# Kernel tuning notes

Hardware: AMD Instinct MI355X
Metric: run time of the kernel (lower is better)

The kernel has to match this reference:

```python
import jax, jax.numpy as jnp
import numpy as np

N = 128       # SSM state size
L = 32768     # l_max / sequence length
DT_MIN, DT_MAX = 0.001, 0.1


def setup_inputs() -> dict:
    key = jax.random.key(0)
    ku, ka, kb, kc, ks = jax.random.split(key, 5)
    u = jax.random.normal(ku, (L,), dtype=jnp.float32)
    # lecun_normal: std = 1/sqrt(fan_in); shift A by -2I for stability over L powers
    A = jax.random.normal(ka, (N, N), dtype=jnp.float32) * (1.0 / np.sqrt(N)) - 2.0 * jnp.eye(N, dtype=jnp.float32)
    B = jax.random.normal(kb, (N, 1), dtype=jnp.float32)            # fan_in=1 -> std 1
    C = jax.random.normal(kc, (1, N), dtype=jnp.float32) * (1.0 / np.sqrt(N))
    D = jnp.ones((1,), dtype=jnp.float32)
    log_step = jax.random.uniform(ks, (1,), dtype=jnp.float32) * (np.log(DT_MAX) - np.log(DT_MIN)) + np.log(DT_MIN)
    return {"u": u, "A": A, "B": B, "C": C, "D": D, "log_step": log_step}


def discretize(a, b, step):
    # bilinear (Tustin) discretization, identical to the flax module
    i = jnp.eye(a.shape[0], dtype=a.dtype)
    bl = jnp.linalg.inv(i - (step / 2.0) * a)
    ab = bl @ (i + (step / 2.0) * a)
    bb = (bl * step) @ b
    return ab, bb


def k_conv(ab, bb, cb, l):
    # K[t] = cb @ ab^t @ bb  -- same math as the matrix_power list-comp,
    # computed with a single scan carrying x_t = ab^t @ bb  (N,1)
    def step(x, _):
        k_t = (cb @ x).reshape(())
        return ab @ x, k_t
    _, k = jax.lax.scan(step, bb, None, length=l)
    return k  # (l,)


def causal_convolution(u, k):
    l = u.shape[0]
    ud = jnp.fft.rfft(jnp.pad(u, (0, k.shape[0])))
    kd = jnp.fft.rfft(jnp.pad(k, (0, l)))
    return jnp.fft.irfft(ud * kd)[:l]


def reference(u, A, B, C, D, log_step):
    step = jnp.exp(log_step)
    ab, bb = discretize(A, B, step)
    K = k_conv(ab, bb, C, u.shape[0])
    return causal_convolution(u, K) + D * u
```

## Files before the change

### kernel.cpp

```cpp
#include <hip/hip_runtime.h>
#include <math.h>

#define L_SEQ 32768
#define NS 128
#define TS 2048

__global__ __launch_bounds__(256) void build_T(const float* __restrict__ A,
                                               const float* __restrict__ lstep,
                                               float* __restrict__ T,
                                               float* __restrict__ U1) {
  int idx = blockIdx.x * 256 + threadIdx.x;
  if (idx >= NS * NS) return;
  int i = idx >> 7, j = idx & 127;
  float step = expf(lstep[0]);
  float alpha = 0.5f * step / (1.0f + step);
  float g = A[idx] + ((i == j) ? 2.0f : 0.0f);
  float t = alpha * g;
  T[idx] = t;
  U1[idx] = t + ((i == j) ? 1.0f : 0.0f);
}

__global__ __launch_bounds__(256) void gemm2(
    const float* __restrict__ A1, const float* __restrict__ B1, float* __restrict__ C1,
    int M1, int lgP1, int ldb1, int ldc1, int mode1,
    const float* __restrict__ A2, const float* __restrict__ B2, float* __restrict__ C2,
    int M2, int lgP2, int ldb2, int ldc2, int mode2,
    int n1, const float* __restrict__ lstep) {
  int b = blockIdx.x;
  bool sec = (b >= n1);
  const float* Ap = sec ? A2 : A1;
  const float* Bp = sec ? B2 : B1;
  float* Cp = sec ? C2 : C1;
  int M   = sec ? M2 : M1;
  int lgP = sec ? lgP2 : lgP1;
  int ldb = sec ? ldb2 : ldb1;
  int ldc = sec ? ldc2 : ldc1;
  int mode = sec ? mode2 : mode1;
  int bid = sec ? (b - n1) : b;

  int idx = bid * 256 + threadIdx.x;
  int total = M << lgP;
  if (idx >= total) return;
  int i = idx >> lgP;
  int j = idx & ((1 << lgP) - 1);

  const float* Arow = Ap + i * NS;
  float acc = 0.f;
#pragma unroll 8
  for (int k = 0; k < NS; ++k) acc = fmaf(Arow[k], Bp[k * ldb + j], acc);

  float out;
  if (mode == 0) {
    out = acc;
  } else if (mode == 1) {
    out = acc + Arow[j];
  } else if (mode == 2) {
    out = acc + Arow[j] + Bp[i * ldb + j] + ((i == j) ? 1.f : 0.f);
  } else {
    float step = expf(lstep[0]);
    out = (2.f / (1.f + step)) * acc - ((i == j) ? 1.f : 0.f);
  }
  Cp[i * ldc + j] = out;
}

__global__ __launch_bounds__(256) void prep(const float* __restrict__ ab,
                                            const float* __restrict__ B,
                                            const float* __restrict__ C,
                                            const float* __restrict__ lstep,
                                            float* __restrict__ R,
                                            float* __restrict__ S) {
  int t = threadIdx.x;
  if (t < NS) {
    float acc = 0.f;
    for (int k = 0; k < NS; ++k) acc = fmaf(ab[t * NS + k], B[k], acc);
    float step = expf(lstep[0]);
    R[t * 256] = 0.5f * step * (acc + B[t]);
  } else if (t < 2 * NS) {
    int j = t - NS;
    S[j] = C[j];
  }
}

__global__ __launch_bounds__(256) void conv_partial(const float* __restrict__ u,
                                                    const float* __restrict__ Kv,
                                                    float* __restrict__ Pp) {
  __shared__ __align__(16) float ks[TS];
  __shared__ __align__(16) float us[2 * TS];

  int bid = blockIdx.x;
  int m = 0;
  while ((m + 1) * (m + 2) / 2 <= bid) m++;
  int c = bid - m * (m + 1) / 2;
  int w0 = (m - c) * TS - TS;
  int tid = threadIdx.x;

  for (int idx = tid; idx < TS; idx += 256) ks[idx] = Kv[c * TS + idx];
  for (int idx = tid; idx < 2 * TS; idx += 256) {
    int gi = w0 + idx;
    us[idx] = (gi >= 0) ? u[gi] : 0.f;
  }
  __syncthreads();

  float acc[8];
#pragma unroll
  for (int i = 0; i < 8; ++i) acc[i] = 0.f;

  int tb = tid << 3;

  for (int s8 = 0; s8 < TS; s8 += 8) {
    float4 k0 = *(const float4*)&ks[s8];
    float4 k1 = *(const float4*)&ks[s8 + 4];
    int base = TS + tb - s8;
    float4 ua = *(const float4*)&us[base - 8];
    float4 ub = *(const float4*)&us[base - 4];
    float4 uc = *(const float4*)&us[base];
    float4 ud = *(const float4*)&us[base + 4];
    float w[16] = {ua.x, ua.y, ua.z, ua.w, ub.x, ub.y, ub.z, ub.w,
                   uc.x, uc.y, uc.z, uc.w, ud.x, ud.y, ud.z, ud.w};
    float kk[8] = {k0.x, k0.y, k0.z, k0.w, k1.x, k1.y, k1.z, k1.w};
#pragma unroll
    for (int ds = 0; ds < 8; ++ds) {
#pragma unroll
      for (int i = 0; i < 8; ++i) acc[i] = fmaf(kk[ds], w[8 + i - ds], acc[i]);
    }
  }

  float* dst = Pp + c * L_SEQ + m * TS + tb;
  *(float4*)&dst[0] = make_float4(acc[0], acc[1], acc[2], acc[3]);
  *(float4*)&dst[4] = make_float4(acc[4], acc[5], acc[6], acc[7]);
}

__global__ __launch_bounds__(256) void reduce_k(const float* __restrict__ Pp,
                                                const float* __restrict__ u,
                                                const float* __restrict__ D,
                                                float* __restrict__ y) {
  int t = blockIdx.x * 256 + threadIdx.x;
  if (t >= L_SEQ) return;
  int mmax = t >> 11;
  float acc = D[0] * u[t];
  for (int c = 0; c <= mmax; ++c) acc += Pp[c * L_SEQ + t];
  y[t] = acc;
}

static inline void launch_gemm1(hipStream_t s, const float* A, const float* B, float* C,
                                int M, int lgP, int ldb, int ldc, int mode,
                                const float* lstep) {
  int n1 = ((M << lgP) + 255) >> 8;
  hipLaunchKernelGGL(gemm2, dim3(n1), dim3(256), 0, s,
                     A, B, C, M, lgP, ldb, ldc, mode,
                     (const float*)nullptr, (const float*)nullptr, (float*)nullptr,
                     0, 0, 0, 0, 0, n1, lstep);
}

static inline void launch_gemm2j(hipStream_t s,
                                 const float* A1, const float* B1, float* C1,
                                 int M1, int lgP1, int ldb1, int ldc1, int mode1,
                                 const float* A2, const float* B2, float* C2,
                                 int M2, int lgP2, int ldb2, int ldc2, int mode2,
                                 const float* lstep) {
  int n1 = ((M1 << lgP1) + 255) >> 8;
  int n2 = ((M2 << lgP2) + 255) >> 8;
  hipLaunchKernelGGL(gemm2, dim3(n1 + n2), dim3(256), 0, s,
                     A1, B1, C1, M1, lgP1, ldb1, ldc1, mode1,
                     A2, B2, C2, M2, lgP2, ldb2, ldc2, mode2, n1, lstep);
}

extern "C" void kernel_launch(void* const* d_in, const int* in_sizes, int n_in,
                              void* d_out, int out_size, void* d_ws, size_t ws_size,
                              hipStream_t stream) {
  (void)in_sizes; (void)n_in; (void)out_size; (void)ws_size;
  const float* u     = (const float*)d_in[0];
  const float* A     = (const float*)d_in[1];
  const float* B     = (const float*)d_in[2];
  const float* C     = (const float*)d_in[3];
  const float* D     = (const float*)d_in[4];
  const float* lstep = (const float*)d_in[5];
  float* y  = (float*)d_out;
  float* ws = (float*)d_ws;

  float* T   = ws + 0;
  float* U1  = ws + 16384;
  float* T2  = ws + 32768;
  float* T4  = ws + 49152;
  float* T8  = ws + 65536;
  float* U12 = ws + 81920;
  float* U48 = ws + 98304;
  float* ab  = ws + 114688;
  float* pwA = ws + 131072;
  float* pwB = ws + 147456;
  float* R   = ws + 163840;
  float* S   = ws + 196608;
  float* Kv  = ws + 212992;
  float* Pp  = ws + 245760;

  hipLaunchKernelGGL(build_T, dim3(64), dim3(256), 0, stream, A, lstep, T, U1);
  launch_gemm1(stream, T, T, T2, 128, 7, 128, 128, 0, lstep);
  launch_gemm2j(stream, T2, T2, T4, 128, 7, 128, 128, 0,
                U1, T2, U12, 128, 7, 128, 128, 1, lstep);
  launch_gemm1(stream, T4, T4, T8, 128, 7, 128, 128, 0, lstep);
  launch_gemm1(stream, T4, T8, U48, 128, 7, 128, 128, 2, lstep);
  launch_gemm1(stream, U12, U48, ab, 128, 7, 128, 128, 3, lstep);
  hipLaunchKernelGGL(prep, dim3(1), dim3(256), 0, stream, ab, B, C, lstep, R, S);

  auto pw = [&](int k) -> float* { return k == 0 ? ab : ((k & 1) ? pwA : pwB); };

  for (int k = 0; k < 8; ++k) {
    launch_gemm2j(stream, pw(k), R, R + (1 << k), 128, k, 256, 256, 0,
                  pw(k), pw(k), pw(k + 1), 128, 7, 128, 128, 0, lstep);
  }
  for (int k = 0; k < 7; ++k) {
    if (k < 6) {
      launch_gemm2j(stream, S, pw(8 + k), S + (1 << k) * 128, 1 << k, 7, 128, 128, 0,
                    pw(8 + k), pw(8 + k), pw(9 + k), 128, 7, 128, 128, 0, lstep);
    } else {
      launch_gemm1(stream, S, pw(8 + k), S + (1 << k) * 128, 1 << k, 7, 128, 128, 0, lstep);
    }
  }

  launch_gemm1(stream, S, R, Kv, 128, 8, 256, 256, 0, lstep);

  hipLaunchKernelGGL(conv_partial, dim3(136), dim3(256), 0, stream, u, Kv, Pp);
  hipLaunchKernelGGL(reduce_k, dim3(128), dim3(256), 0, stream, Pp, u, D, y);
}
```

Baseline: 245.9 us.

## Fuse matrix-power chain into one persistent kernel with grid barriers; retile convolution

Replaces the roughly twenty small GEMM launches that build the discretized matrix, its powers and the kernel vector with one persistent 128-block kernel. The stages are separated by atomic-counter grid barriers, so per-launch overhead and inter-kernel gaps go away. The block convolution drops from 2048 to 1024 tiles (528 blocks, four outputs per thread) and uses an XOR-swizzled shared-memory layout for u with a register-rotating window. The grid barrier assumes all 128 blocks are co-resident, and the reduce step now sums more partial blocks per output.

New measurement: 277.7 us. 1.13x slower.

```diff
diff --git a/kernel.cpp b/kernel.cpp
--- a/kernel.cpp
+++ b/kernel.cpp
@@ -2,132 +2,205 @@
 #include <math.h>
 
 #define L_SEQ 32768
-#define NS 128
-#define TS 2048
-
-__global__ __launch_bounds__(256) void build_T(const float* __restrict__ A,
+#define NBLK 128
+
+__device__ __forceinline__ void gbar(int* cnt, int target) {
+  __syncthreads();
+  if (threadIdx.x == 0) {
+    __hip_atomic_fetch_add(cnt, 1, __ATOMIC_RELEASE, __HIP_MEMORY_SCOPE_AGENT);
+    while (__hip_atomic_load(cnt, __ATOMIC_ACQUIRE, __HIP_MEMORY_SCOPE_AGENT) < target) {
+      __builtin_amdgcn_s_sleep(2);
+    }
+  }
+  __syncthreads();
+}
+
+__device__ __forceinline__ float dot128(const float* __restrict__ Ar,
+                                        const float* __restrict__ B,
+                                        int ldb, int j) {
+  float a0 = 0.f, a1 = 0.f, a2 = 0.f, a3 = 0.f;
+#pragma unroll
+  for (int k = 0; k < 128; k += 4) {
+    a0 = fmaf(Ar[k],     B[(k)     * ldb + j], a0);
+    a1 = fmaf(Ar[k + 1], B[(k + 1) * ldb + j], a1);
+    a2 = fmaf(Ar[k + 2], B[(k + 2) * ldb + j], a2);
+    a3 = fmaf(Ar[k + 3], B[(k + 3) * ldb + j], a3);
+  }
+  return (a0 + a1) + (a2 + a3);
+}
+
+__global__ __launch_bounds__(256) void chain_k(const float* __restrict__ A,
+                                               const float* __restrict__ Bv,
+                                               const float* __restrict__ Cv,
                                                const float* __restrict__ lstep,
-                                               float* __restrict__ T,
-                                               float* __restrict__ U1) {
-  int idx = blockIdx.x * 256 + threadIdx.x;
-  if (idx >= NS * NS) return;
-  int i = idx >> 7, j = idx & 127;
+                                               float* ws) {
+  int* cnt   = (int*)ws;
+  float* T   = ws + 16;
+  float* U1  = T   + 16384;
+  float* T2  = U1  + 16384;
+  float* T4  = T2  + 16384;
+  float* T8  = T4  + 16384;
+  float* U12 = T8  + 16384;
+  float* U48 = U12 + 16384;
+  float* ab  = U48 + 16384;
+  float* pwA = ab  + 16384;
+  float* pwB = pwA + 16384;
+  float* R   = pwB + 16384;
+  float* S   = R   + 32768;
+  float* Kv  = S   + 16384;
+
+  int tid = blockIdx.x * 256 + threadIdx.x;
   float step = expf(lstep[0]);
-  float alpha = 0.5f * step / (1.0f + step);
-  float g = A[idx] + ((i == j) ? 2.0f : 0.0f);
-  float t = alpha * g;
-  T[idx] = t;
-  U1[idx] = t + ((i == j) ? 1.0f : 0.0f);
-}
-
-__global__ __launch_bounds__(256) void gemm2(
-    const float* __restrict__ A1, const float* __restrict__ B1, float* __restrict__ C1,
-    int M1, int lgP1, int ldb1, int ldc1, int mode1,
-    const float* __restrict__ A2, const float* __restrict__ B2, float* __restrict__ C2,
-    int M2, int lgP2, int ldb2, int ldc2, int mode2,
-    int n1, const float* __restrict__ lstep) {
-  int b = blockIdx.x;
-  bool sec = (b >= n1);
-  const float* Ap = sec ? A2 : A1;
-  const float* Bp = sec ? B2 : B1;
-  float* Cp = sec ? C2 : C1;
-  int M   = sec ? M2 : M1;
-  int lgP = sec ? lgP2 : lgP1;
-  int ldb = sec ? ldb2 : ldb1;
-  int ldc = sec ? ldc2 : ldc1;
-  int mode = sec ? mode2 : mode1;
-  int bid = sec ? (b - n1) : b;
-
-  int idx = bid * 256 + threadIdx.x;
-  int total = M << lgP;
-  if (idx >= total) return;
-  int i = idx >> lgP;
-  int j = idx & ((1 << lgP) - 1);
-
-  const float* Arow = Ap + i * NS;
-  float acc = 0.f;
-#pragma unroll 8
-  for (int k = 0; k < NS; ++k) acc = fmaf(Arow[k], Bp[k * ldb + j], acc);
-
-  float out;
-  if (mode == 0) {
-    out = acc;
-  } else if (mode == 1) {
-    out = acc + Arow[j];
-  } else if (mode == 2) {
-    out = acc + Arow[j] + Bp[i * ldb + j] + ((i == j) ? 1.f : 0.f);
+  int bar = 0;
+
+  if (tid < 16384) {
+    int i = tid >> 7, j = tid & 127;
+    float alpha = 0.5f * step / (1.0f + step);
+    float g = A[tid] + ((i == j) ? 2.0f : 0.0f);
+    float t = alpha * g;
+    T[tid] = t;
+    U1[tid] = t + ((i == j) ? 1.0f : 0.0f);
+  }
+  gbar(cnt, NBLK * (++bar));
+
+  if (tid < 16384) {
+    int i = tid >> 7, j = tid & 127;
+    T2[tid] = dot128(T + i * 128, T, 128, j);
+  }
+  gbar(cnt, NBLK * (++bar));
+
+  if (tid < 16384) {
+    int i = tid >> 7, j = tid & 127;
+    T4[tid] = dot128(T2 + i * 128, T2, 128, j);
   } else {
-    float step = expf(lstep[0]);
-    out = (2.f / (1.f + step)) * acc - ((i == j) ? 1.f : 0.f);
-  }
-  Cp[i * ldc + j] = out;
-}
-
-__global__ __launch_bounds__(256) void prep(const float* __restrict__ ab,
-                                            const float* __restrict__ B,
-                                            const float* __restrict__ C,
-                                            const float* __restrict__ lstep,
-                                            float* __restrict__ R,
-                                            float* __restrict__ S) {
-  int t = threadIdx.x;
-  if (t < NS) {
+    int t2 = tid - 16384;
+    int i = t2 >> 7, j = t2 & 127;
+    U12[t2] = dot128(U1 + i * 128, T2, 128, j) + U1[t2];
+  }
+  gbar(cnt, NBLK * (++bar));
+
+  if (tid < 16384) {
+    int i = tid >> 7, j = tid & 127;
+    T8[tid] = dot128(T4 + i * 128, T4, 128, j);
+  }
+  gbar(cnt, NBLK * (++bar));
+
+  if (tid < 16384) {
+    int i = tid >> 7, j = tid & 127;
+    U48[tid] = dot128(T4 + i * 128, T8, 128, j) + T4[tid] + T8[tid] +
+               ((i == j) ? 1.f : 0.f);
+  }
+  gbar(cnt, NBLK * (++bar));
+
+  if (tid < 16384) {
+    int i = tid >> 7, j = tid & 127;
+    ab[tid] = (2.f / (1.f + step)) * dot128(U12 + i * 128, U48, 128, j) -
+              ((i == j) ? 1.f : 0.f);
+  }
+  gbar(cnt, NBLK * (++bar));
+
+  if (tid < 128) {
     float acc = 0.f;
-    for (int k = 0; k < NS; ++k) acc = fmaf(ab[t * NS + k], B[k], acc);
-    float step = expf(lstep[0]);
-    R[t * 256] = 0.5f * step * (acc + B[t]);
-  } else if (t < 2 * NS) {
-    int j = t - NS;
-    S[j] = C[j];
-  }
-}
-
-__global__ __launch_bounds__(256) void conv_partial(const float* __restrict__ u,
-                                                    const float* __restrict__ Kv,
-                                                    float* __restrict__ Pp) {
-  __shared__ __align__(16) float ks[TS];
-  __shared__ __align__(16) float us[2 * TS];
-
-  int bid = blockIdx.x;
+    for (int k = 0; k < 128; ++k) acc = fmaf(ab[tid * 128 + k], Bv[k], acc);
+    R[tid * 256] = 0.5f * step * (acc + Bv[tid]);
+  } else if (tid < 256) {
+    S[tid - 128] = Cv[tid - 128];
+  }
+  gbar(cnt, NBLK * (++bar));
+
+  for (int k = 0; k < 8; ++k) {
+    const float* pwk = (k == 0) ? ab : ((k & 1) ? pwA : pwB);
+    float* pwn = ((k + 1) & 1) ? pwA : pwB;
+    if (tid < (128 << k)) {
+      int i = tid >> k, j = tid & ((1 << k) - 1);
+      R[i * 256 + (1 << k) + j] = dot128(pwk + i * 128, R, 256, j);
+    } else if (tid >= 16384) {
+      int t2 = tid - 16384;
+      int i = t2 >> 7, j = t2 & 127;
+      pwn[t2] = dot128(pwk + i * 128, pwk, 128, j);
+    }
+    gbar(cnt, NBLK * (++bar));
+  }
+
+  for (int k = 0; k < 7; ++k) {
+    const float* pwk = ((8 + k) & 1) ? pwA : pwB;
+    float* pwn = ((9 + k) & 1) ? pwA : pwB;
+    if (tid < (128 << k)) {
+      int i = tid >> 7, j = tid & 127;
+      S[((1 << k) + i) * 128 + j] = dot128(S + i * 128, pwk, 128, j);
+    } else if (k < 6 && tid >= 16384) {
+      int t2 = tid - 16384;
+      int i = t2 >> 7, j = t2 & 127;
+      pwn[t2] = dot128(pwk + i * 128, pwk, 128, j);
+    }
+    gbar(cnt, NBLK * (++bar));
+  }
+
+  {
+    int t1 = tid >> 8, t0 = tid & 255;
+    Kv[tid] = dot128(S + t1 * 128, R, 256, t0);
+  }
+}
+
+__global__ __launch_bounds__(256) void conv_k(const float* __restrict__ u,
+                                              const float* __restrict__ Kv,
+                                              float* __restrict__ Pp) {
+  __shared__ __align__(16) float ks[1024];
+  __shared__ __align__(16) float usw[2048];
+
+  int bid = blockIdx.x, tid = threadIdx.x;
   int m = 0;
   while ((m + 1) * (m + 2) / 2 <= bid) m++;
   int c = bid - m * (m + 1) / 2;
-  int w0 = (m - c) * TS - TS;
-  int tid = threadIdx.x;
-
-  for (int idx = tid; idx < TS; idx += 256) ks[idx] = Kv[c * TS + idx];
-  for (int idx = tid; idx < 2 * TS; idx += 256) {
+  int w0 = (m - c - 1) << 10;
+
+  for (int idx = tid; idx < 1024; idx += 256) ks[idx] = Kv[(c << 10) + idx];
+  for (int idx = tid; idx < 2048; idx += 256) {
     int gi = w0 + idx;
-    us[idx] = (gi >= 0) ? u[gi] : 0.f;
+    float v = (gi >= 0) ? u[gi] : 0.f;
+    int b = idx >> 2;
+    int pb = b ^ ((b >> 3) & 7);
+    usw[(pb << 2) | (idx & 3)] = v;
   }
   __syncthreads();
 
-  float acc[8];
-#pragma unroll
-  for (int i = 0; i < 8; ++i) acc[i] = 0.f;
-
-  int tb = tid << 3;
-
-  for (int s8 = 0; s8 < TS; s8 += 8) {
-    float4 k0 = *(const float4*)&ks[s8];
-    float4 k1 = *(const float4*)&ks[s8 + 4];
-    int base = TS + tb - s8;
-    float4 ua = *(const float4*)&us[base - 8];
-    float4 ub = *(const float4*)&us[base - 4];
-    float4 uc = *(const float4*)&us[base];
-    float4 ud = *(const float4*)&us[base + 4];
-    float w[16] = {ua.x, ua.y, ua.z, ua.w, ub.x, ub.y, ub.z, ub.w,
-                   uc.x, uc.y, uc.z, uc.w, ud.x, ud.y, ud.z, ud.w};
-    float kk[8] = {k0.x, k0.y, k0.z, k0.w, k1.x, k1.y, k1.z, k1.w};
-#pragma unroll
-    for (int ds = 0; ds < 8; ++ds) {
-#pragma unroll
-      for (int i = 0; i < 8; ++i) acc[i] = fmaf(kk[ds], w[8 + i - ds], acc[i]);
-    }
-  }
-
-  float* dst = Pp + c * L_SEQ + m * TS + tb;
-  *(float4*)&dst[0] = make_float4(acc[0], acc[1], acc[2], acc[3]);
-  *(float4*)&dst[4] = make_float4(acc[4], acc[5], acc[6], acc[7]);
+  int tb = tid << 2;
+
+#define LD4(x)                                                      \
+  (*(const float4*)&usw[((((x) >> 2) ^ ((((x) >> 2) >> 3) & 7)) << 2)])
+
+  float4 wlo = LD4(1020 + tb);
+  float4 whi = LD4(1024 + tb);
+  float acc0 = 0.f, acc1 = 0.f, acc2 = 0.f, acc3 = 0.f;
+
+#pragma unroll 4
+  for (int s8 = 0; s8 < 1024; s8 += 4) {
+    float4 k4 = *(const float4*)&ks[s8];
+    acc0 = fmaf(k4.x, whi.x, acc0);
+    acc0 = fmaf(k4.y, wlo.w, acc0);
+    acc0 = fmaf(k4.z, wlo.z, acc0);
+    acc0 = fmaf(k4.w, wlo.y, acc0);
+    acc1 = fmaf(k4.x, whi.y, acc1);
+    acc1 = fmaf(k4.y, whi.x, acc1);
+    acc1 = fmaf(k4.z, wlo.w, acc1);
+    acc1 = fmaf(k4.w, wlo.z, acc1);
+    acc2 = fmaf(k4.x, whi.z, acc2);
+    acc2 = fmaf(k4.y, whi.y, acc2);
+    acc2 = fmaf(k4.z, whi.x, acc2);
+    acc2 = fmaf(k4.w, wlo.w, acc2);
+    acc3 = fmaf(k4.x, whi.w, acc3);
+    acc3 = fmaf(k4.y, whi.z, acc3);
+    acc3 = fmaf(k4.z, whi.y, acc3);
+    acc3 = fmaf(k4.w, whi.x, acc3);
+    if (s8 < 1020) {
+      whi = wlo;
+      wlo = LD4(1016 + tb - s8);
+    }
+  }
+#undef LD4
+
+  float* dst = Pp + (c << 15) + (m << 10) + tb;
+  *(float4*)dst = make_float4(acc0, acc1, acc2, acc3);
 }
 
 __global__ __launch_bounds__(256) void reduce_k(const float* __restrict__ Pp,
@@ -136,33 +209,10 @@
                                                 float* __restrict__ y) {
   int t = blockIdx.x * 256 + threadIdx.x;
   if (t >= L_SEQ) return;
-  int mmax = t >> 11;
+  int mm = t >> 10;
   float acc = D[0] * u[t];
-  for (int c = 0; c <= mmax; ++c) acc += Pp[c * L_SEQ + t];
+  for (int c = 0; c <= mm; ++c) acc += Pp[(c << 15) + t];
   y[t] = acc;
-}
-
-static inline void launch_gemm1(hipStream_t s, const float* A, const float* B, float* C,
-                                int M, int lgP, int ldb, int ldc, int mode,
-                                const float* lstep) {
-  int n1 = ((M << lgP) + 255) >> 8;
-  hipLaunchKernelGGL(gemm2, dim3(n1), dim3(256), 0, s,
-                     A, B, C, M, lgP, ldb, ldc, mode,
-                     (const float*)nullptr, (const float*)nullptr, (float*)nullptr,
-                     0, 0, 0, 0, 0, n1, lstep);
-}
-
-static inline void launch_gemm2j(hipStream_t s,
-                                 const float* A1, const float* B1, float* C1,
-                                 int M1, int lgP1, int ldb1, int ldc1, int mode1,
-                                 const float* A2, const float* B2, float* C2,
-                                 int M2, int lgP2, int ldb2, int ldc2, int mode2,
-                                 const float* lstep) {
-  int n1 = ((M1 << lgP1) + 255) >> 8;
-  int n2 = ((M2 << lgP2) + 255) >> 8;
-  hipLaunchKernelGGL(gemm2, dim3(n1 + n2), dim3(256), 0, s,
-                     A1, B1, C1, M1, lgP1, ldb1, ldc1, mode1,
-                     A2, B2, C2, M2, lgP2, ldb2, ldc2, mode2, n1, lstep);
 }
 
 extern "C" void kernel_launch(void* const* d_in, const int* in_sizes, int n_in,
@@ -178,47 +228,11 @@
   float* y  = (float*)d_out;
   float* ws = (float*)d_ws;
 
-  float* T   = ws + 0;
-  float* U1  = ws + 16384;
-  float* T2  = ws + 32768;
-  float* T4  = ws + 49152;
-  float* T8  = ws + 65536;
-  float* U12 = ws + 81920;
-  float* U48 = ws + 98304;
-  float* ab  = ws + 114688;
-  float* pwA = ws + 131072;
-  float* pwB = ws + 147456;
-  float* R   = ws + 163840;
-  float* S   = ws + 196608;
-  float* Kv  = ws + 212992;
-  float* Pp  = ws + 245760;
-
-  hipLaunchKernelGGL(build_T, dim3(64), dim3(256), 0, stream, A, lstep, T, U1);
-  launch_gemm1(stream, T, T, T2, 128, 7, 128, 128, 0, lstep);
-  launch_gemm2j(stream, T2, T2, T4, 128, 7, 128, 128, 0,
-                U1, T2, U12, 128, 7, 128, 128, 1, lstep);
-  launch_gemm1(stream, T4, T4, T8, 128, 7, 128, 128, 0, lstep);
-  launch_gemm1(stream, T4, T8, U48, 128, 7, 128, 128, 2, lstep);
-  launch_gemm1(stream, U12, U48, ab, 128, 7, 128, 128, 3, lstep);
-  hipLaunchKernelGGL(prep, dim3(1), dim3(256), 0, stream, ab, B, C, lstep, R, S);
-
-  auto pw = [&](int k) -> float* { return k == 0 ? ab : ((k & 1) ? pwA : pwB); };
-
-  for (int k = 0; k < 8; ++k) {
-    launch_gemm2j(stream, pw(k), R, R + (1 << k), 128, k, 256, 256, 0,
-                  pw(k), pw(k), pw(k + 1), 128, 7, 128, 128, 0, lstep);
-  }
-  for (int k = 0; k < 7; ++k) {
-    if (k < 6) {
-      launch_gemm2j(stream, S, pw(8 + k), S + (1 << k) * 128, 1 << k, 7, 128, 128, 0,
-                    pw(8 + k), pw(8 + k), pw(9 + k), 128, 7, 128, 128, 0, lstep);
-    } else {
-      launch_gemm1(stream, S, pw(8 + k), S + (1 << k) * 128, 1 << k, 7, 128, 128, 0, lstep);
-    }
-  }
-
-  launch_gemm1(stream, S, R, Kv, 128, 8, 256, 256, 0, lstep);
-
-  hipLaunchKernelGGL(conv_partial, dim3(136), dim3(256), 0, stream, u, Kv, Pp);
-  hipLaunchKernelGGL(reduce_k, dim3(128), dim3(256), 0, stream, Pp, u, D, y);
-}
+  float* Kv = ws + 16 + 10 * 16384 + 32768 + 16384;
+  float* Pp = Kv + 32768;
+
+  hipMemsetAsync(d_ws, 0, 64, stream);
+  hipLaunchKernelGGL(chain_k, dim3(NBLK), dim3(256), 0, stream, A, B, C, lstep, ws);
+  hipLaunchKernelGGL(conv_k, dim3(528), dim3(256), 0, stream, u, Kv, Pp);
+  hipLaunchKernelGGL(reduce_k, dim3(L_SEQ / 256), dim3(256), 0, stream, Pp, u, D, y);
+}
```
